# Kernel optimization log

Measured on AMD Instinct MI355X. Metric: run time of the kernel, lower is better.

The kernel has to match this reference:

```python
import jax, jax.numpy as jnp
import numpy as np

EPS = 1e-12  # torch F.normalize clamps the norm at 1e-12

def _l2norm(v, axis):
    n = jnp.sqrt(jnp.sum(v * v, axis=axis, keepdims=True))
    return v / jnp.maximum(n, EPS)

def setup_inputs() -> dict:
    key = jax.random.key(0)
    k1, k2, k3, k4 = jax.random.split(key, 4)
    N, C, H, W, K = 64, 64, 64, 64, 128
    alpha = 1.0
    x = jax.random.normal(k1, (N, C, H, W), dtype=jnp.float32)
    centroids = jax.random.uniform(k2, (K, C), dtype=jnp.float32)
    # conv is initialized from centroids (2*alpha*c, -alpha*||c||) but is an
    # independent parameter after init; keep the init relationship for realism.
    conv_w = 2.0 * alpha * centroids
    conv_b = -alpha * jnp.sqrt(jnp.sum(centroids * centroids, axis=1))
    return {"x": x, "centroids": centroids, "conv_w": conv_w, "conv_b": conv_b}

def reference(x, centroids, conv_w, conv_b):
    N, C, H, W = x.shape
    K = centroids.shape[0]
    # L2-normalize descriptors along channel dim
    xn = _l2norm(x, axis=1)                                   # [N,C,H,W]
    # 1x1 conv == per-pixel linear map C->K
    logits = jnp.einsum('nchw,kc->nkhw', xn, conv_w) + conv_b[None, :, None, None]
    sa = jax.nn.softmax(logits.reshape(N, K, H * W), axis=1)  # [N,K,HW]
    xf = xn.reshape(N, C, H * W)                              # [N,C,HW]
    # vlad[n,k,c] = sum_l sa[n,k,l] * (xf[n,c,l] - centroids[k,c])
    #            = (sa @ xf^T)[n,k,c] - sum_l sa[n,k,l] * centroids[k,c]
    vlad = jnp.einsum('nkl,ncl->nkc', sa, xf) - sa.sum(axis=-1)[:, :, None] * centroids[None]
    vlad = _l2norm(vlad, axis=2)            # intra-normalization per cluster
    vlad = vlad.reshape(N, K * C)
    vlad = _l2norm(vlad, axis=1)            # global L2 normalization
    return vlad
```

## Files before the change

kernel.cpp:

```cpp
#include <hip/hip_runtime.h>
#include <math.h>

#define NIMG   64
#define CDIM   64
#define HWPX   4096
#define KCL    128
#define TL     32
#define SHIFT  10.0f
#define RSQRT128 0.08838834764831845f

#define XP_S 72
#define XC_S 40
#define PH_S 40

typedef __attribute__((ext_vector_type(8))) short short8;
typedef __attribute__((ext_vector_type(4))) float f32x4;

#define MFMA(a, b, c) __builtin_amdgcn_mfma_f32_16x16x32_bf16((a), (b), (c), 0, 0, 0)

__device__ __forceinline__ void tsplit(float f, short& hs, short& ls) {
    unsigned u = __builtin_bit_cast(unsigned, f);
    hs = (short)(u >> 16);
    float hf = __builtin_bit_cast(float, u & 0xffff0000u);
    ls = (short)(__builtin_bit_cast(unsigned, f - hf) >> 16);
}
__device__ __forceinline__ short f2bf(float f) {
    unsigned u = __builtin_bit_cast(unsigned, f);
    return (short)((u + 0x7fffu + ((u >> 16) & 1u)) >> 16);
}

template <int NP>
__global__ __launch_bounds__(256, 2)
void netvlad_main(const float* __restrict__ x,
                  const float* __restrict__ conv_w,
                  const float* __restrict__ conv_b,
                  float* __restrict__ vout,
                  float* __restrict__ asout,
                  int use_atomic)
{
    constexpr int PIXPART = HWPX / NP;
    constexpr int NCHUNK  = PIXPART / TL;

    __shared__ __align__(16) short xp_hi[TL * XP_S], xp_lo[TL * XP_S];
    __shared__ __align__(16) short xc[CDIM * XC_S];
    __shared__ __align__(16) short ph[KCL * PH_S];
    __shared__ float redA[4 * 33];
    __shared__ float sumP[4 * TL];

    const int t   = threadIdx.x;
    const int w   = t >> 6;
    const int l   = t & 63;
    const int l15 = l & 15, l4 = l >> 4;
    const int n    = blockIdx.x / NP;
    const int part = blockIdx.x - n * NP;
    const int p_s  = t & 31;
    const int sg   = t >> 5;

    short8 wh[2][2], wl[2][2];
    #pragma unroll
    for (int kt = 0; kt < 2; ++kt) {
        const int krow = (2 * w + kt) * 16 + l15;
        #pragma unroll
        for (int ks = 0; ks < 2; ++ks) {
            const float4* wp = (const float4*)(conv_w + krow * CDIM + ks * 32 + l4 * 8);
            float4 wa = wp[0], wb = wp[1];
            float wv[8] = {wa.x, wa.y, wa.z, wa.w, wb.x, wb.y, wb.z, wb.w};
            #pragma unroll
            for (int j = 0; j < 8; ++j) {
                short hs, ls; tsplit(wv[j], hs, ls);
                wh[kt][ks][j] = hs; wl[kt][ks][j] = ls;
            }
        }
    }
    float cbr[2][4];
    #pragma unroll
    for (int kt = 0; kt < 2; ++kt)
        #pragma unroll
        for (int i = 0; i < 4; ++i)
            cbr[kt][i] = conv_b[(2 * w + kt) * 16 + l4 * 4 + i] - SHIFT;

    f32x4 acc2[2][4];
    #pragma unroll
    for (int a = 0; a < 2; ++a)
        #pragma unroll
        for (int b = 0; b < 4; ++b) acc2[a][b] = (f32x4)0.0f;
    float asr[2][4];
    #pragma unroll
    for (int a = 0; a < 2; ++a)
        #pragma unroll
        for (int i = 0; i < 4; ++i) asr[a][i] = 0.f;

    const float* xbase = x + (size_t)n * CDIM * HWPX + part * PIXPART;

    float xv[8];
    #pragma unroll
    for (int j = 0; j < 8; ++j)
        xv[j] = xbase[(sg * 8 + j) * HWPX + p_s];

    for (int ch = 0; ch < NCHUNK; ++ch) {
        float ssq = 0.f;
        #pragma unroll
        for (int j = 0; j < 8; ++j) ssq += xv[j] * xv[j];
        ssq += __shfl_xor(ssq, 32);
        if (l < 32) redA[w * 33 + p_s] = ssq;

        short8 vh, vl;
        #pragma unroll
        for (int j = 0; j < 8; ++j) {
            short hs, ls; tsplit(xv[j], hs, ls);
            vh[j] = hs; vl[j] = ls;
            xc[(sg * 8 + j) * XC_S + p_s] = f2bf(xv[j]);
        }
        *(short8*)&xp_hi[p_s * XP_S + sg * 8] = vh;
        *(short8*)&xp_lo[p_s * XP_S + sg * 8] = vl;
        __syncthreads();

        if (ch + 1 < NCHUNK) {
            #pragma unroll
            for (int j = 0; j < 8; ++j)
                xv[j] = xbase[(sg * 8 + j) * HWPX + (ch + 1) * TL + p_s];
        }

        f32x4 a1[2][2];
        #pragma unroll
        for (int a = 0; a < 2; ++a)
            #pragma unroll
            for (int b = 0; b < 2; ++b) a1[a][b] = (f32x4)0.0f;
        #pragma unroll
        for (int ks = 0; ks < 2; ++ks) {
            #pragma unroll
            for (int pt = 0; pt < 2; ++pt) {
                short8 bh = *(short8*)&xp_hi[(pt * 16 + l15) * XP_S + ks * 32 + l4 * 8];
                short8 bl = *(short8*)&xp_lo[(pt * 16 + l15) * XP_S + ks * 32 + l4 * 8];
                #pragma unroll
                for (int kt = 0; kt < 2; ++kt) {
                    a1[kt][pt] = MFMA(wh[kt][ks], bh, a1[kt][pt]);
                    a1[kt][pt] = MFMA(wh[kt][ks], bl, a1[kt][pt]);
                    a1[kt][pt] = MFMA(wl[kt][ks], bh, a1[kt][pt]);
                }
            }
        }

        float rn[2];
        #pragma unroll
        for (int pt = 0; pt < 2; ++pt) {
            const int col = pt * 16 + l15;
            float s0 = redA[col] + redA[33 + col];
            float s1 = redA[2 * 33 + col] + redA[3 * 33 + col];
            rn[pt] = 1.0f / fmaxf(sqrtf(s0 + s1), 1e-12f);
        }

        float e[2][2][4], sp[2] = {0.f, 0.f};
        #pragma unroll
        for (int kt = 0; kt < 2; ++kt)
            #pragma unroll
            for (int pt = 0; pt < 2; ++pt)
                #pragma unroll
                for (int i = 0; i < 4; ++i) {
                    float ev = __expf(fmaf(a1[kt][pt][i], rn[pt], cbr[kt][i]));
                    e[kt][pt][i] = ev;
                    sp[pt] += ev;
                }
        #pragma unroll
        for (int pt = 0; pt < 2; ++pt) {
            sp[pt] += __shfl_xor(sp[pt], 16);
            sp[pt] += __shfl_xor(sp[pt], 32);
        }
        if (l4 == 0) {
            sumP[w * TL + l15]      = sp[0];
            sumP[w * TL + 16 + l15] = sp[1];
        }
        __syncthreads();

        float rden[2], rdn2[2];
        #pragma unroll
        for (int pt = 0; pt < 2; ++pt) {
            const int col = pt * 16 + l15;
            float den = sumP[col] + sumP[TL + col] + sumP[2 * TL + col] + sumP[3 * TL + col];
            rden[pt] = 1.0f / den;
            rdn2[pt] = rden[pt] * rn[pt];
        }

        #pragma unroll
        for (int kt = 0; kt < 2; ++kt)
            #pragma unroll
            for (int i = 0; i < 4; ++i) {
                const int row = (2 * w + kt) * 16 + l4 * 4 + i;
                #pragma unroll
                for (int pt = 0; pt < 2; ++pt) {
                    float ev = e[kt][pt][i];
                    asr[kt][i] = fmaf(ev, rden[pt], asr[kt][i]);
                    ph[row * PH_S + pt * 16 + l15] = f2bf(ev * rdn2[pt]);
                }
            }

        {
            short8 xh2[4];
            #pragma unroll
            for (int ct = 0; ct < 4; ++ct)
                xh2[ct] = *(short8*)&xc[(ct * 16 + l15) * XC_S + l4 * 8];
            #pragma unroll
            for (int kt = 0; kt < 2; ++kt) {
                short8 ah = *(short8*)&ph[((2 * w + kt) * 16 + l15) * PH_S + l4 * 8];
                #pragma unroll
                for (int ct = 0; ct < 4; ++ct)
                    acc2[kt][ct] = MFMA(ah, xh2[ct], acc2[kt][ct]);
            }
        }
        __syncthreads();
    }

    float* vg = use_atomic ? vout + (size_t)n * KCL * CDIM
                           : vout + (size_t)blockIdx.x * KCL * CDIM;
    #pragma unroll
    for (int kt = 0; kt < 2; ++kt)
        #pragma unroll
        for (int ct = 0; ct < 4; ++ct)
            #pragma unroll
            for (int i = 0; i < 4; ++i) {
                const int row = (2 * w + kt) * 16 + l4 * 4 + i;
                const int col = ct * 16 + l15;
                if (use_atomic) atomicAdd(&vg[row * CDIM + col], acc2[kt][ct][i]);
                else            vg[row * CDIM + col] = acc2[kt][ct][i];
            }

    #pragma unroll
    for (int kt = 0; kt < 2; ++kt)
        #pragma unroll
        for (int i = 0; i < 4; ++i) {
            float v = asr[kt][i];
            v += __shfl_xor(v, 1); v += __shfl_xor(v, 2);
            v += __shfl_xor(v, 4); v += __shfl_xor(v, 8);
            if (l15 == 0) {
                const int row = (2 * w + kt) * 16 + l4 * 4 + i;
                if (use_atomic) atomicAdd(&asout[n * KCL + row], v);
                else            asout[blockIdx.x * KCL + row] = v;
            }
        }
}

__global__ __launch_bounds__(256)
void netvlad_finalize(const float* __restrict__ vpart,
                      const float* __restrict__ aspart,
                      const float* __restrict__ cent,
                      float* __restrict__ out,
                      int nparts)
{
    const int t = threadIdx.x;
    const int n  = blockIdx.x >> 3;
    const int kg = blockIdx.x & 7;
    const int k  = kg * 16 + (t >> 4);
    const int c0 = (t & 15) * 4;

    float vsum[4] = {0.f, 0.f, 0.f, 0.f};
    float av = 0.f;
    for (int pt = 0; pt < nparts; ++pt) {
        const float* vg = vpart + (((size_t)n * nparts + pt) * KCL + k) * CDIM + c0;
        float4 a = *(const float4*)vg;
        vsum[0] += a.x; vsum[1] += a.y; vsum[2] += a.z; vsum[3] += a.w;
        av += aspart[(n * nparts + pt) * KCL + k];
    }

    float4 cq = *(const float4*)(cent + k * CDIM + c0);
    float cc[4] = {cq.x, cq.y, cq.z, cq.w};
    float ss = 0.f;
    #pragma unroll
    for (int j = 0; j < 4; ++j) {
        vsum[j] -= av * cc[j];
        ss += vsum[j] * vsum[j];
    }
    ss += __shfl_xor(ss, 1); ss += __shfl_xor(ss, 2);
    ss += __shfl_xor(ss, 4); ss += __shfl_xor(ss, 8);
    const float s = (1.0f / fmaxf(sqrtf(ss), 1e-12f)) * RSQRT128;

    float4 o;
    o.x = vsum[0] * s; o.y = vsum[1] * s; o.z = vsum[2] * s; o.w = vsum[3] * s;
    *(float4*)(out + (size_t)n * KCL * CDIM + k * CDIM + c0) = o;
}

extern "C" void kernel_launch(void* const* d_in, const int* in_sizes, int n_in,
                              void* d_out, int out_size, void* d_ws, size_t ws_size,
                              hipStream_t stream) {
    const float* x     = (const float*)d_in[0];
    const float* cent  = (const float*)d_in[1];
    const float* convw = (const float*)d_in[2];
    const float* convb = (const float*)d_in[3];
    float* out = (float*)d_out;

    const size_t need16 = (size_t)NIMG * 16 * (KCL * CDIM + KCL) * sizeof(float);
    const size_t need8  = (size_t)NIMG * 8  * (KCL * CDIM + KCL) * sizeof(float);

    if (ws_size >= need16) {
        float* vws  = (float*)d_ws;
        float* asws = vws + (size_t)NIMG * 16 * KCL * CDIM;
        netvlad_main<16><<<dim3(NIMG * 16), dim3(256), 0, stream>>>(
            x, convw, convb, vws, asws, 0);
        netvlad_finalize<<<dim3(NIMG * 8), dim3(256), 0, stream>>>(
            vws, asws, cent, out, 16);
    } else if (ws_size >= need8) {
        float* vws  = (float*)d_ws;
        float* asws = vws + (size_t)NIMG * 8 * KCL * CDIM;
        netvlad_main<8><<<dim3(NIMG * 8), dim3(256), 0, stream>>>(
            x, convw, convb, vws, asws, 0);
        netvlad_finalize<<<dim3(NIMG * 8), dim3(256), 0, stream>>>(
            vws, asws, cent, out, 8);
    } else {
        float* vws  = (float*)d_ws;
        float* asws = vws + (size_t)NIMG * KCL * CDIM;
        const size_t zb = (size_t)NIMG * (KCL * CDIM + KCL) * sizeof(float);
        hipMemsetAsync(d_ws, 0, zb, stream);
        netvlad_main<8><<<dim3(NIMG * 8), dim3(256), 0, stream>>>(
            x, convw, convb, vws, asws, 1);
        netvlad_finalize<<<dim3(NIMG * 8), dim3(256), 0, stream>>>(
            vws, asws, cent, out, 1);
    }
}
```

Measured before the change: 131.3 us.

## Use packed bf16 conversions and drop the 16-way pixel split path

Replaces the scalar float-to-bf16 split and round helpers with packed operations: v_perm assembles the hi/lo halves two at a time, and the v_cvt_pk_bf16_f32 instruction does the rounding conversion for the xc and ph tiles. The aim is fewer ALU instructions in the per-chunk staging loop. The launcher also removes the NP=16 configuration, so the main kernel now runs with 8 partitions per image even when the workspace would fit 16. That halves the grid size and doubles the per-block work, which trades partial-sum traffic and finalize reads against parallelism.

```diff
diff --git a/kernel.cpp b/kernel.cpp
--- a/kernel.cpp
+++ b/kernel.cpp
@@ -18,16 +18,7 @@
 
 #define MFMA(a, b, c) __builtin_amdgcn_mfma_f32_16x16x32_bf16((a), (b), (c), 0, 0, 0)
 
-__device__ __forceinline__ void tsplit(float f, short& hs, short& ls) {
-    unsigned u = __builtin_bit_cast(unsigned, f);
-    hs = (short)(u >> 16);
-    float hf = __builtin_bit_cast(float, u & 0xffff0000u);
-    ls = (short)(__builtin_bit_cast(unsigned, f - hf) >> 16);
-}
-__device__ __forceinline__ short f2bf(float f) {
-    unsigned u = __builtin_bit_cast(unsigned, f);
-    return (short)((u + 0x7fffu + ((u >> 16) & 1u)) >> 16);
-}
+#define PERM_HI16 0x07060302u
 
 template <int NP>
 __global__ __launch_bounds__(256, 2)
@@ -67,8 +58,10 @@
             float wv[8] = {wa.x, wa.y, wa.z, wa.w, wb.x, wb.y, wb.z, wb.w};
             #pragma unroll
             for (int j = 0; j < 8; ++j) {
-                short hs, ls; tsplit(wv[j], hs, ls);
-                wh[kt][ks][j] = hs; wl[kt][ks][j] = ls;
+                unsigned u = __builtin_bit_cast(unsigned, wv[j]);
+                wh[kt][ks][j] = (short)(u >> 16);
+                float hf = __builtin_bit_cast(float, u & 0xffff0000u);
+                wl[kt][ks][j] = (short)(__builtin_bit_cast(unsigned, wv[j] - hf) >> 16);
             }
         }
     }
@@ -104,15 +97,29 @@
         ssq += __shfl_xor(ssq, 32);
         if (l < 32) redA[w * 33 + p_s] = ssq;
 
-        short8 vh, vl;
-        #pragma unroll
-        for (int j = 0; j < 8; ++j) {
-            short hs, ls; tsplit(xv[j], hs, ls);
-            vh[j] = hs; vl[j] = ls;
-            xc[(sg * 8 + j) * XC_S + p_s] = f2bf(xv[j]);
-        }
-        *(short8*)&xp_hi[p_s * XP_S + sg * 8] = vh;
-        *(short8*)&xp_lo[p_s * XP_S + sg * 8] = vl;
+        unsigned uh[4], ul[4];
+        #pragma unroll
+        for (int jp = 0; jp < 4; ++jp) {
+            const unsigned u0 = __builtin_bit_cast(unsigned, xv[2 * jp]);
+            const unsigned u1 = __builtin_bit_cast(unsigned, xv[2 * jp + 1]);
+            uh[jp] = __builtin_amdgcn_perm(u1, u0, PERM_HI16);
+            const float h0 = __builtin_bit_cast(float, u0 & 0xffff0000u);
+            const float h1 = __builtin_bit_cast(float, u1 & 0xffff0000u);
+            const unsigned lo0 = __builtin_bit_cast(unsigned, xv[2 * jp] - h0);
+            const unsigned lo1 = __builtin_bit_cast(unsigned, xv[2 * jp + 1] - h1);
+            ul[jp] = __builtin_amdgcn_perm(lo1, lo0, PERM_HI16);
+        }
+        *(uint4*)&xp_hi[p_s * XP_S + sg * 8] = make_uint4(uh[0], uh[1], uh[2], uh[3]);
+        *(uint4*)&xp_lo[p_s * XP_S + sg * 8] = make_uint4(ul[0], ul[1], ul[2], ul[3]);
+
+        #pragma unroll
+        for (int jp = 0; jp < 4; ++jp) {
+            unsigned pk;
+            asm("v_cvt_pk_bf16_f32 %0, %1, %2"
+                : "=v"(pk) : "v"(xv[2 * jp]), "v"(xv[2 * jp + 1]));
+            xc[(sg * 8 + 2 * jp)     * XC_S + p_s] = (short)pk;
+            xc[(sg * 8 + 2 * jp + 1) * XC_S + p_s] = (short)(pk >> 16);
+        }
         __syncthreads();
 
         if (ch + 1 < NCHUNK) {
@@ -186,12 +193,14 @@
             #pragma unroll
             for (int i = 0; i < 4; ++i) {
                 const int row = (2 * w + kt) * 16 + l4 * 4 + i;
-                #pragma unroll
-                for (int pt = 0; pt < 2; ++pt) {
-                    float ev = e[kt][pt][i];
-                    asr[kt][i] = fmaf(ev, rden[pt], asr[kt][i]);
-                    ph[row * PH_S + pt * 16 + l15] = f2bf(ev * rdn2[pt]);
-                }
+                const float e0 = e[kt][0][i], e1 = e[kt][1][i];
+                asr[kt][i] = fmaf(e0, rden[0], asr[kt][i]);
+                asr[kt][i] = fmaf(e1, rden[1], asr[kt][i]);
+                const float p0 = e0 * rdn2[0], p1 = e1 * rdn2[1];
+                unsigned pk;
+                asm("v_cvt_pk_bf16_f32 %0, %1, %2" : "=v"(pk) : "v"(p0), "v"(p1));
+                ph[row * PH_S + l15]      = (short)pk;
+                ph[row * PH_S + 16 + l15] = (short)(pk >> 16);
             }
 
         {
@@ -287,17 +296,9 @@
     const float* convb = (const float*)d_in[3];
     float* out = (float*)d_out;
 
-    const size_t need16 = (size_t)NIMG * 16 * (KCL * CDIM + KCL) * sizeof(float);
-    const size_t need8  = (size_t)NIMG * 8  * (KCL * CDIM + KCL) * sizeof(float);
-
-    if (ws_size >= need16) {
-        float* vws  = (float*)d_ws;
-        float* asws = vws + (size_t)NIMG * 16 * KCL * CDIM;
-        netvlad_main<16><<<dim3(NIMG * 16), dim3(256), 0, stream>>>(
-            x, convw, convb, vws, asws, 0);
-        netvlad_finalize<<<dim3(NIMG * 8), dim3(256), 0, stream>>>(
-            vws, asws, cent, out, 16);
-    } else if (ws_size >= need8) {
+    const size_t need8 = (size_t)NIMG * 8 * (KCL * CDIM + KCL) * sizeof(float);
+
+    if (ws_size >= need8) {
         float* vws  = (float*)d_ws;
         float* asws = vws + (size_t)NIMG * 8 * KCL * CDIM;
         netvlad_main<8><<<dim3(NIMG * 8), dim3(256), 0, stream>>>(
```

Measured after the change: 127.3 us. 1.03x faster.
